# Kernel optimization log

Hardware: AMD Instinct MI355X
Metric: run time of the kernel (lower is better)

The kernel has to match this reference:

```python
import jax, jax.numpy as jnp
import numpy as np

B, T, V = 4, 2048, 2048
D, H, L = 512, 8, 4
HD = D // H


def setup_inputs() -> dict:
    key = jax.random.key(0)
    ks = jax.random.split(key, 8)
    inp = {
        "x": jax.random.normal(ks[0], (B, T, V), dtype=jnp.float32),
        "token_embedding": jax.random.normal(ks[1], (D, V), dtype=jnp.float32),
        "position_embedding": jax.random.normal(ks[2], (T, D), dtype=jnp.float32),
        "Wk": jax.random.normal(ks[3], (L, D, D), dtype=jnp.float32),
        "Wq": jax.random.normal(ks[4], (L, D, D), dtype=jnp.float32),
        "Wv": jax.random.normal(ks[5], (L, D, D), dtype=jnp.float32),
        "Wp": jax.random.normal(ks[6], (L, D, D), dtype=jnp.float32),
        "readout": jax.random.normal(ks[7], (V, D), dtype=jnp.float32),
    }
    return inp


def _attention_block(h, wk, wq, wv, wp):
    # h: [B, T, D]; weights [D, D] (inner_dim == D since head_dim*num_heads == D)
    b, t, c = h.shape
    s = c ** (-0.5)

    def proj(w):
        # F.linear(h, w) = h @ w.T -> [B,T,D] -> [B,H,T,HD], scaled by C^{-1/2}
        return (jnp.einsum('btc,dc->btd', h, w) * s).reshape(b, t, H, HD).transpose(0, 2, 1, 3)

    q, k, v = proj(wq), proj(wk), proj(wv)
    scores = jnp.einsum('bhqd,bhkd->bhqk', q, k) * (HD ** (-0.5))  # [B,H,T,T]
    attn = jax.nn.softmax(scores, axis=-1)
    out = jnp.einsum('bhqk,bhkd->bhqd', attn, v)  # [B,H,T,HD]
    out = out.transpose(0, 2, 1, 3).reshape(b, t, c)
    # projection.size(-1) == inner_dim == D
    return jnp.einsum('btc,oc->bto', out, wp) * (c ** (-0.5))


def reference(x, token_embedding, position_embedding, Wk, Wq, Wv, Wp, readout):
    b, t, c = x.shape  # c == vocab_size
    tok = jnp.einsum('btv,dv->btd', x, token_embedding) * (c ** (-0.5))
    h = tok + position_embedding[:t]
    for l in range(L):
        h = _attention_block(h, Wk[l], Wq[l], Wv[l], Wp[l])
    # logits on last token; readout.size(-1) == D
    logits = jnp.einsum('bd,vd->bv', h[:, -1, :], readout) * (D ** (-0.5))
    return logits
```

## Files before the change

### kernel.cpp

```cpp
#include <hip/hip_runtime.h>
#include <math.h>

typedef __attribute__((ext_vector_type(4))) float    f32x4;
typedef __attribute__((ext_vector_type(2))) _Float16 f16x2;
typedef __attribute__((ext_vector_type(4))) _Float16 f16x4;
typedef __attribute__((ext_vector_type(8))) _Float16 f16x8;

constexpr int Bc  = 4;
constexpr int Tc  = 2048;
constexpr int Vc  = 2048;
constexpr int Dc  = 512;
constexpr int Hc  = 8;
constexpr int HDc = 64;
constexpr int Lc  = 4;
constexpr size_t SZe = (size_t)Bc * Tc * Dc;

constexpr float SM_C = 12.0f;

__device__ __forceinline__ void gload_lds16(const _Float16* g, _Float16* s) {
    __builtin_amdgcn_global_load_lds(
        (const __attribute__((address_space(1))) void*)g,
        (__attribute__((address_space(3))) void*)s,
        16, 0, 0);
}

__device__ __forceinline__ f16x2 cvt_pk(float a, float b) {
    return __builtin_bit_cast(f16x2, __builtin_amdgcn_cvt_pkrtz(a, b));
}

__global__ __launch_bounds__(256) void cvt_k(
    const float* __restrict__ in, _Float16* __restrict__ out, int n4)
{
    for (int i = blockIdx.x * 256 + threadIdx.x; i < n4; i += gridDim.x * 256) {
        float4 v = ((const float4*)in)[i];
        f16x4 h = {(_Float16)v.x, (_Float16)v.y, (_Float16)v.z, (_Float16)v.w};
        *(f16x4*)&out[(size_t)i * 4] = h;
    }
}

__global__ __launch_bounds__(256) void cvtW_k(
    const float* __restrict__ a, const float* __restrict__ b,
    const float* __restrict__ c, const float* __restrict__ d,
    _Float16* __restrict__ oa, _Float16* __restrict__ ob,
    _Float16* __restrict__ oc, _Float16* __restrict__ od, int n4)
{
    const float* in; _Float16* out;
    switch (blockIdx.y) {
        case 0:  in = a; out = oa; break;
        case 1:  in = b; out = ob; break;
        case 2:  in = c; out = oc; break;
        default: in = d; out = od; break;
    }
    for (int i = blockIdx.x * 256 + threadIdx.x; i < n4; i += gridDim.x * 256) {
        float4 v = ((const float4*)in)[i];
        f16x4 h = {(_Float16)v.x, (_Float16)v.y, (_Float16)v.z, (_Float16)v.w};
        *(f16x4*)&out[(size_t)i * 4] = h;
    }
}

template<bool QKV>
__global__ __launch_bounds__(256) void gemm_f16(
    const _Float16* __restrict__ A,
    const _Float16* __restrict__ W0, const _Float16* __restrict__ W1,
    const _Float16* __restrict__ W2,
    void* __restrict__ C0, const float* __restrict__ pos,
    int K, float scA, float scB)
{
    __shared__ __align__(16) _Float16 LA[2][128 * 64];
    __shared__ __align__(16) _Float16 LB[2][128 * 64];

    const int tid = threadIdx.x;
    const int w  = tid >> 6, l = tid & 63;
    const int li = l & 15,  lg = l >> 4;
    const int wm = w >> 1,  wn = w & 1;
    const int m0 = blockIdx.x * 128;

    int sec = 0, n0;
    const _Float16* Wb;
    if (QKV) {
        sec = blockIdx.y >> 2; n0 = (blockIdx.y & 3) * 128;
        Wb = (sec == 0) ? W0 : ((sec == 1) ? W1 : W2);
    } else {
        n0 = blockIdx.y * 128; Wb = W0;
    }
    const float scale = (sec == 0) ? scA : scB;

    const _Float16* srcA[4];
    const _Float16* srcB[4];
#pragma unroll
    for (int i = 0; i < 4; ++i) {
        const int d = i * 4096 + tid * 16;
        const int r = d >> 7, cb = (d & 127) ^ ((r & 7) << 4);
        srcA[i] = A  + (size_t)(m0 + r) * K + (cb >> 1);
        srcB[i] = Wb + (size_t)(n0 + r) * K + (cb >> 1);
    }

    auto stage = [&](int b) {
#pragma unroll
        for (int i = 0; i < 4; ++i) { gload_lds16(srcA[i], &LA[b][i * 2048 + tid * 8]); srcA[i] += 64; }
#pragma unroll
        for (int i = 0; i < 4; ++i) { gload_lds16(srcB[i], &LB[b][i * 2048 + tid * 8]); srcB[i] += 64; }
    };

    f32x4 acc[4][4];
#pragma unroll
    for (int i = 0; i < 4; ++i)
#pragma unroll
        for (int j = 0; j < 4; ++j) acc[i][j] = (f32x4){0.f, 0.f, 0.f, 0.f};

    auto compute = [&](int b) {
        const char* Ab = (const char*)&LA[b][0];
        const char* Bb = (const char*)&LB[b][0];
        f16x8 af[4][2], bf[4][2];
#pragma unroll
        for (int mb = 0; mb < 4; ++mb) {
            const int row = wm * 64 + mb * 16 + li, sz = (row & 7) << 4;
#pragma unroll
            for (int fi = 0; fi < 2; ++fi)
                af[mb][fi] = *(const f16x8*)(Ab + row * 128 + ((fi * 64 + lg * 16) ^ sz));
        }
#pragma unroll
        for (int nb = 0; nb < 4; ++nb) {
            const int row = wn * 64 + nb * 16 + li, sz = (row & 7) << 4;
#pragma unroll
            for (int fi = 0; fi < 2; ++fi)
                bf[nb][fi] = *(const f16x8*)(Bb + row * 128 + ((fi * 64 + lg * 16) ^ sz));
        }
#pragma unroll
        for (int mb = 0; mb < 4; ++mb)
#pragma unroll
            for (int nb = 0; nb < 4; ++nb)
#pragma unroll
                for (int fi = 0; fi < 2; ++fi)
                    acc[mb][nb] = __builtin_amdgcn_mfma_f32_16x16x32_f16(
                        af[mb][fi], bf[nb][fi], acc[mb][nb], 0, 0, 0);
    };

    const int NTk = K >> 6;
    stage(0);
    for (int kt = 0; kt < NTk; ++kt) {
        const int cur = kt & 1;
        if (kt + 1 < NTk) {
            stage(cur ^ 1);
            asm volatile("s_waitcnt vmcnt(8)" ::: "memory");
        } else {
            asm volatile("s_waitcnt vmcnt(0)" ::: "memory");
        }
        __builtin_amdgcn_s_barrier();
        __builtin_amdgcn_sched_barrier(0);
        compute(cur);
        __builtin_amdgcn_s_barrier();
        __builtin_amdgcn_sched_barrier(0);
    }

#pragma unroll
    for (int mb = 0; mb < 4; ++mb) {
#pragma unroll
        for (int nb = 0; nb < 4; ++nb) {
            const int mbase = m0 + wm * 64 + mb * 16 + lg * 4;
            const int nc    = n0 + wn * 64 + nb * 16 + li;
            if (QKV && sec == 2) {
                const int bb2 = mbase >> 11, t0 = mbase & (Tc - 1);
                const int hh2 = nc >> 6,     dd = nc & 63;
                f16x4 vv;
#pragma unroll
                for (int r = 0; r < 4; ++r) vv[r] = (_Float16)(acc[mb][nb][r] * scale);
                _Float16* vt = (_Float16*)C0 + 2 * SZe;
                *(f16x4*)&vt[(((size_t)bb2 * Hc + hh2) * HDc + dd) * Tc + t0] = vv;
            } else if (QKV) {
                _Float16* outp = (_Float16*)C0 + (size_t)sec * SZe;
#pragma unroll
                for (int r = 0; r < 4; ++r) {
                    const int m = mbase + r, bb2 = m >> 11, t = m & (Tc - 1);
                    outp[(((size_t)bb2 * Hc + (nc >> 6)) * Tc + t) * HDc + (nc & 63)] =
                        (_Float16)(acc[mb][nb][r] * scale);
                }
            } else {
                _Float16* outp = (_Float16*)C0;
#pragma unroll
                for (int r = 0; r < 4; ++r) {
                    const int m = mbase + r;
                    float val = acc[mb][nb][r] * scale;
                    if (pos) val += pos[(size_t)(m & (Tc - 1)) * Dc + nc];
                    outp[(size_t)m * Dc + nc] = (_Float16)val;
                }
            }
        }
    }
}

__global__ __launch_bounds__(256) void attn_mfma(
    const _Float16* __restrict__ Qh, const _Float16* __restrict__ Kh,
    const _Float16* __restrict__ Vt, _Float16* __restrict__ o)
{
    __shared__ __align__(16) _Float16 Ks[2][64 * 64];
    __shared__ __align__(16) _Float16 Vs[2][64 * 64];

    const int bid = blockIdx.x;
    const int bh  = bid & 31;
    const int qt  = bid >> 5;
    const int hh  = bh & (Hc - 1);
    const int bb  = bh >> 3;
    const int w   = threadIdx.x >> 6;
    const int l   = threadIdx.x & 63;
    const int li  = l & 15, lg = l >> 4;
    const int q0  = qt * 64 + w * 16;
    const int swz = (li & 7) << 4;

    const _Float16* Qb = Qh + (size_t)bh * Tc * HDc;
    const _Float16* Kb = Kh + (size_t)bh * Tc * HDc;
    const _Float16* Vb = Vt + (size_t)bh * HDc * Tc;

    f16x8 qf[2];
#pragma unroll
    for (int fi = 0; fi < 2; ++fi)
        qf[fi] = *(const f16x8*)&Qb[(size_t)(q0 + li) * HDc + fi * 32 + lg * 8];

    const int off0 = w * 2048 + l * 16;
    const int off1 = off0 + 1024;
    const int r0 = off0 >> 7, cs0 = (off0 & 127) ^ ((r0 & 7) << 4);
    const int r1 = off1 >> 7, cs1 = (off1 & 127) ^ ((r1 & 7) << 4);
    const _Float16* sK0 = Kb + r0 * HDc + (cs0 >> 1);
    const _Float16* sK1 = Kb + r1 * HDc + (cs1 >> 1);
    const _Float16* sV0 = Vb + (size_t)r0 * Tc + (cs0 >> 1);
    const _Float16* sV1 = Vb + (size_t)r1 * Tc + (cs1 >> 1);

    auto stage = [&](int b) {
        gload_lds16(sK0, &Ks[b][w * 1024]);
        gload_lds16(sK1, &Ks[b][w * 1024 + 512]);
        gload_lds16(sV0, &Vs[b][w * 1024]);
        gload_lds16(sV1, &Vs[b][w * 1024 + 512]);
        sK0 += 64 * HDc; sK1 += 64 * HDc;
        sV0 += 64;       sV1 += 64;
    };

    f32x4 oacc[4];
#pragma unroll
    for (int dt = 0; dt < 4; ++dt) oacc[dt] = (f32x4){0.f, 0.f, 0.f, 0.f};
    f32x4 lacc = (f32x4){0.f, 0.f, 0.f, 0.f};
    const f16x4 ones = (f16x4){(_Float16)1.f, (_Float16)1.f, (_Float16)1.f, (_Float16)1.f};

    stage(0);
    constexpr int NT = Tc / 64;
    for (int kt = 0; kt < NT; ++kt) {
        const int cur = kt & 1;
        if (kt + 1 < NT) {
            stage(cur ^ 1);
            asm volatile("s_waitcnt vmcnt(4)" ::: "memory");
        } else {
            asm volatile("s_waitcnt vmcnt(0)" ::: "memory");
        }
        __builtin_amdgcn_s_barrier();
        __builtin_amdgcn_sched_barrier(0);

        const char* KL = (const char*)&Ks[cur][0];
        const char* VL = (const char*)&Vs[cur][0];

        f32x4 s[4];
        __builtin_amdgcn_s_setprio(1);
#pragma unroll
        for (int t = 0; t < 4; ++t) {
            s[t] = (f32x4){-SM_C, -SM_C, -SM_C, -SM_C};
            const char* kr = KL + (t * 16 + li) * 128;
#pragma unroll
            for (int fi = 0; fi < 2; ++fi) {
                f16x8 kf = *(const f16x8*)(kr + ((fi * 64 + lg * 16) ^ swz));
                s[t] = __builtin_amdgcn_mfma_f32_16x16x32_f16(kf, qf[fi], s[t], 0, 0, 0);
            }
        }
        __builtin_amdgcn_s_setprio(0);

        f16x4 pf[4];
#pragma unroll
        for (int t = 0; t < 4; ++t) {
            float p0 = __builtin_amdgcn_exp2f(s[t][0]);
            float p1 = __builtin_amdgcn_exp2f(s[t][1]);
            float p2 = __builtin_amdgcn_exp2f(s[t][2]);
            float p3 = __builtin_amdgcn_exp2f(s[t][3]);
            f16x2 lo = cvt_pk(p0, p1);
            f16x2 hi = cvt_pk(p2, p3);
            pf[t] = (f16x4){lo[0], lo[1], hi[0], hi[1]};
        }

        __builtin_amdgcn_s_setprio(1);
#pragma unroll
        for (int t = 0; t < 4; ++t)
            lacc = __builtin_amdgcn_mfma_f32_16x16x16f16(ones, pf[t], lacc, 0, 0, 0);
#pragma unroll
        for (int dt = 0; dt < 4; ++dt) {
            const char* vr = VL + (dt * 16 + li) * 128;
#pragma unroll
            for (int t = 0; t < 4; ++t) {
                f16x4 vf = *(const f16x4*)(vr + ((t * 32 + lg * 8) ^ swz));
                oacc[dt] = __builtin_amdgcn_mfma_f32_16x16x16f16(vf, pf[t], oacc[dt], 0, 0, 0);
            }
        }
        __builtin_amdgcn_s_setprio(0);

        __builtin_amdgcn_s_barrier();
        __builtin_amdgcn_sched_barrier(0);
    }

    const float inv = 1.f / lacc[0];
    _Float16* op = o + ((size_t)(bb * Tc + q0 + li) * Dc + hh * HDc + lg * 4);
#pragma unroll
    for (int dt = 0; dt < 4; ++dt) {
        f16x4 rv = {(_Float16)(oacc[dt][0] * inv), (_Float16)(oacc[dt][1] * inv),
                    (_Float16)(oacc[dt][2] * inv), (_Float16)(oacc[dt][3] * inv)};
        *(f16x4*)(op + dt * 16) = rv;
    }
}

__global__ __launch_bounds__(256) void readout_k(
    const _Float16* __restrict__ h, const float* __restrict__ ro,
    float* __restrict__ out, float scale)
{
    const int idx = blockIdx.x * 256 + threadIdx.x;
    const int vv  = idx & (Vc - 1);
    const int bb  = idx >> 11;
    const _Float16* hp = h + (size_t)(bb * Tc + (Tc - 1)) * Dc;
    const float* rp = ro + (size_t)vv * Dc;
    float ax = 0.f, ay = 0.f, az = 0.f, aw = 0.f;
#pragma unroll 8
    for (int i = 0; i < Dc / 4; ++i) {
        f16x4  hv = *(const f16x4*)(hp + i * 4);
        float4 rv = *(const float4*)(rp + i * 4);
        ax = fmaf((float)hv[0], rv.x, ax);
        ay = fmaf((float)hv[1], rv.y, ay);
        az = fmaf((float)hv[2], rv.z, az);
        aw = fmaf((float)hv[3], rv.w, aw);
    }
    out[idx] = ((ax + ay) + (az + aw)) * scale;
}

extern "C" void kernel_launch(void* const* d_in, const int* in_sizes, int n_in,
                              void* d_out, int out_size, void* d_ws, size_t ws_size,
                              hipStream_t stream)
{
    const float* x    = (const float*)d_in[0];
    const float* temb = (const float*)d_in[1];
    const float* pemb = (const float*)d_in[2];
    const float* Wk   = (const float*)d_in[3];
    const float* Wq   = (const float*)d_in[4];
    const float* Wv   = (const float*)d_in[5];
    const float* Wp   = (const float*)d_in[6];
    const float* ro   = (const float*)d_in[7];
    float* out = (float*)d_out;

    _Float16* h16    = (_Float16*)d_ws;
    _Float16* temb16 = h16 + SZe;
    _Float16* wq16   = temb16 + (size_t)Dc * Vc;
    _Float16* wk16   = wq16 + (size_t)Lc * Dc * Dc;
    _Float16* wv16   = wk16 + (size_t)Lc * Dc * Dc;
    _Float16* wp16   = wv16 + (size_t)Lc * Dc * Dc;
    _Float16* o16    = wp16 + (size_t)Lc * Dc * Dc;
    _Float16* qh     = o16 + SZe;
    _Float16* kh     = qh + SZe;
    _Float16* vt     = kh + SZe;
    _Float16* x16    = o16;

    const float s_emb  = 1.0f / sqrtf((float)Vc);
    const float s_proj = 1.0f / sqrtf((float)Dc);
    const float s_q    = s_proj * 0.125f * 1.44269504f;

    const int W4 = Lc * Dc * Dc / 4;
    cvt_k<<<2048, 256, 0, stream>>>(x, x16, (int)SZe);
    cvt_k<<<512, 256, 0, stream>>>(temb, temb16, Dc * Vc / 4);
    cvtW_k<<<dim3(512, 4), 256, 0, stream>>>(Wq, Wk, Wv, Wp,
                                             wq16, wk16, wv16, wp16, W4);

    gemm_f16<false><<<dim3(64, 4), 256, 0, stream>>>(
        x16, temb16, nullptr, nullptr, h16, pemb, Vc, s_emb, s_emb);

    const size_t WOFF = (size_t)Dc * Dc;
    for (int lyr = 0; lyr < Lc; ++lyr) {
        gemm_f16<true><<<dim3(64, 12), 256, 0, stream>>>(
            h16, wq16 + lyr * WOFF, wk16 + lyr * WOFF, wv16 + lyr * WOFF,
            qh, nullptr, Dc, s_q, s_proj);

        attn_mfma<<<Bc * Hc * (Tc / 64), 256, 0, stream>>>(qh, kh, vt, o16);

        gemm_f16<false><<<dim3(64, 4), 256, 0, stream>>>(
            o16, wp16 + lyr * WOFF, nullptr, nullptr, h16, nullptr, Dc, s_proj, s_proj);
    }

    readout_k<<<(Bc * Vc) / 256, 256, 0, stream>>>(h16, ro, out, s_proj);
}
```

Baseline: 454.3 us.

## Store K/V in MFMA-fragment order and shrink GEMM N-tile to 64

The QKV GEMM epilogue now writes K and V directly in a pre-tiled layout that matches the MFMA fragment order, so attention stages contiguous 16-byte chunks into LDS and reads fragments with simple linear offsets, with no XOR swizzle. Each V fragment read is now one 8-wide load split into two MFMA operands. Separately, the GEMM tile shrinks from 128x128 to 128x64, doubling the grid in N to raise occupancy and block count. The smaller tile gives less reuse per block, and the scattered scalar K stores in the epilogue may coalesce less well.

Result: faster. 409.9 us (-9.8%).

```diff
diff --git a/kernel.cpp b/kernel.cpp
--- a/kernel.cpp
+++ b/kernel.cpp
@@ -58,6 +58,7 @@
     }
 }
 
+
 template<bool QKV>
 __global__ __launch_bounds__(256) void gemm_f16(
     const _Float16* __restrict__ A,
@@ -67,7 +68,7 @@
     int K, float scA, float scB)
 {
     __shared__ __align__(16) _Float16 LA[2][128 * 64];
-    __shared__ __align__(16) _Float16 LB[2][128 * 64];
+    __shared__ __align__(16) _Float16 LB[2][64 * 64];
 
     const int tid = threadIdx.x;
     const int w  = tid >> 6, l = tid & 63;
@@ -78,20 +79,25 @@
     int sec = 0, n0;
     const _Float16* Wb;
     if (QKV) {
-        sec = blockIdx.y >> 2; n0 = (blockIdx.y & 3) * 128;
+        sec = blockIdx.y >> 3; n0 = (blockIdx.y & 7) * 64;
         Wb = (sec == 0) ? W0 : ((sec == 1) ? W1 : W2);
     } else {
-        n0 = blockIdx.y * 128; Wb = W0;
+        n0 = blockIdx.y * 64; Wb = W0;
     }
     const float scale = (sec == 0) ? scA : scB;
 
     const _Float16* srcA[4];
-    const _Float16* srcB[4];
+    const _Float16* srcB[2];
 #pragma unroll
     for (int i = 0; i < 4; ++i) {
         const int d = i * 4096 + tid * 16;
         const int r = d >> 7, cb = (d & 127) ^ ((r & 7) << 4);
-        srcA[i] = A  + (size_t)(m0 + r) * K + (cb >> 1);
+        srcA[i] = A + (size_t)(m0 + r) * K + (cb >> 1);
+    }
+#pragma unroll
+    for (int i = 0; i < 2; ++i) {
+        const int d = i * 4096 + tid * 16;
+        const int r = d >> 7, cb = (d & 127) ^ ((r & 7) << 4);
         srcB[i] = Wb + (size_t)(n0 + r) * K + (cb >> 1);
     }
 
@@ -99,19 +105,19 @@
 #pragma unroll
         for (int i = 0; i < 4; ++i) { gload_lds16(srcA[i], &LA[b][i * 2048 + tid * 8]); srcA[i] += 64; }
 #pragma unroll
-        for (int i = 0; i < 4; ++i) { gload_lds16(srcB[i], &LB[b][i * 2048 + tid * 8]); srcB[i] += 64; }
+        for (int i = 0; i < 2; ++i) { gload_lds16(srcB[i], &LB[b][i * 2048 + tid * 8]); srcB[i] += 64; }
     };
 
-    f32x4 acc[4][4];
+    f32x4 acc[4][2];
 #pragma unroll
     for (int i = 0; i < 4; ++i)
 #pragma unroll
-        for (int j = 0; j < 4; ++j) acc[i][j] = (f32x4){0.f, 0.f, 0.f, 0.f};
+        for (int j = 0; j < 2; ++j) acc[i][j] = (f32x4){0.f, 0.f, 0.f, 0.f};
 
     auto compute = [&](int b) {
         const char* Ab = (const char*)&LA[b][0];
         const char* Bb = (const char*)&LB[b][0];
-        f16x8 af[4][2], bf[4][2];
+        f16x8 af[4][2], bf[2][2];
 #pragma unroll
         for (int mb = 0; mb < 4; ++mb) {
             const int row = wm * 64 + mb * 16 + li, sz = (row & 7) << 4;
@@ -120,8 +126,8 @@
                 af[mb][fi] = *(const f16x8*)(Ab + row * 128 + ((fi * 64 + lg * 16) ^ sz));
         }
 #pragma unroll
-        for (int nb = 0; nb < 4; ++nb) {
-            const int row = wn * 64 + nb * 16 + li, sz = (row & 7) << 4;
+        for (int nb = 0; nb < 2; ++nb) {
+            const int row = wn * 32 + nb * 16 + li, sz = (row & 7) << 4;
 #pragma unroll
             for (int fi = 0; fi < 2; ++fi)
                 bf[nb][fi] = *(const f16x8*)(Bb + row * 128 + ((fi * 64 + lg * 16) ^ sz));
@@ -129,7 +135,7 @@
 #pragma unroll
         for (int mb = 0; mb < 4; ++mb)
 #pragma unroll
-            for (int nb = 0; nb < 4; ++nb)
+            for (int nb = 0; nb < 2; ++nb)
 #pragma unroll
                 for (int fi = 0; fi < 2; ++fi)
                     acc[mb][nb] = __builtin_amdgcn_mfma_f32_16x16x32_f16(
@@ -142,7 +148,7 @@
         const int cur = kt & 1;
         if (kt + 1 < NTk) {
             stage(cur ^ 1);
-            asm volatile("s_waitcnt vmcnt(8)" ::: "memory");
+            asm volatile("s_waitcnt vmcnt(6)" ::: "memory");
         } else {
             asm volatile("s_waitcnt vmcnt(0)" ::: "memory");
         }
@@ -156,19 +162,32 @@
 #pragma unroll
     for (int mb = 0; mb < 4; ++mb) {
 #pragma unroll
-        for (int nb = 0; nb < 4; ++nb) {
+        for (int nb = 0; nb < 2; ++nb) {
             const int mbase = m0 + wm * 64 + mb * 16 + lg * 4;
-            const int nc    = n0 + wn * 64 + nb * 16 + li;
+            const int nc    = n0 + wn * 32 + nb * 16 + li;
             if (QKV && sec == 2) {
-                const int bb2 = mbase >> 11, t0 = mbase & (Tc - 1);
-                const int hh2 = nc >> 6,     dd = nc & 63;
+                const int t = mbase & (Tc - 1);
+                const int bh2 = (mbase >> 11) * Hc + (nc >> 6), d = nc & 63;
                 f16x4 vv;
 #pragma unroll
                 for (int r = 0; r < 4; ++r) vv[r] = (_Float16)(acc[mb][nb][r] * scale);
-                _Float16* vt = (_Float16*)C0 + 2 * SZe;
-                *(f16x4*)&vt[(((size_t)bb2 * Hc + hh2) * HDc + dd) * Tc + t0] = vv;
+                _Float16* vf = (_Float16*)C0 + 2 * SZe;
+                const size_t adr =
+                    (((size_t)bh2 * 32 + (t >> 6)) * 8 + ((d >> 4) & 3) * 2 + ((t >> 5) & 1)) * 512
+                    + ((d & 15) + 16 * ((t >> 2) & 3)) * 8 + ((t >> 4) & 1) * 4;
+                *(f16x4*)&vf[adr] = vv;
+            } else if (QKV && sec == 1) {
+                _Float16* kf = (_Float16*)C0 + SZe;
+                const int t0 = mbase & (Tc - 1);
+                const int bh2 = (mbase >> 11) * Hc + (nc >> 6), d = nc & 63;
+                const size_t adr0 =
+                    (((size_t)bh2 * 32 + (t0 >> 6)) * 8 + ((t0 >> 4) & 3) * 2 + (d >> 5)) * 512
+                    + ((t0 & 15) + 16 * ((d >> 3) & 3)) * 8 + (d & 7);
+#pragma unroll
+                for (int r = 0; r < 4; ++r)
+                    kf[adr0 + (size_t)r * 8] = (_Float16)(acc[mb][nb][r] * scale);
             } else if (QKV) {
-                _Float16* outp = (_Float16*)C0 + (size_t)sec * SZe;
+                _Float16* outp = (_Float16*)C0;
 #pragma unroll
                 for (int r = 0; r < 4; ++r) {
                     const int m = mbase + r, bb2 = m >> 11, t = m & (Tc - 1);
@@ -190,48 +209,41 @@
 }
 
 __global__ __launch_bounds__(256) void attn_mfma(
-    const _Float16* __restrict__ Qh, const _Float16* __restrict__ Kh,
-    const _Float16* __restrict__ Vt, _Float16* __restrict__ o)
-{
-    __shared__ __align__(16) _Float16 Ks[2][64 * 64];
-    __shared__ __align__(16) _Float16 Vs[2][64 * 64];
+    const _Float16* __restrict__ Qh, const _Float16* __restrict__ Kf,
+    const _Float16* __restrict__ Vf, _Float16* __restrict__ o)
+{
+    __shared__ __align__(16) _Float16 Ks[2][4096];
+    __shared__ __align__(16) _Float16 Vs[2][4096];
 
     const int bid = blockIdx.x;
     const int bh  = bid & 31;
     const int qt  = bid >> 5;
     const int hh  = bh & (Hc - 1);
     const int bb  = bh >> 3;
-    const int w   = threadIdx.x >> 6;
-    const int l   = threadIdx.x & 63;
+    const int tid = threadIdx.x;
+    const int w   = tid >> 6;
+    const int l   = tid & 63;
     const int li  = l & 15, lg = l >> 4;
     const int q0  = qt * 64 + w * 16;
-    const int swz = (li & 7) << 4;
 
     const _Float16* Qb = Qh + (size_t)bh * Tc * HDc;
-    const _Float16* Kb = Kh + (size_t)bh * Tc * HDc;
-    const _Float16* Vb = Vt + (size_t)bh * HDc * Tc;
 
     f16x8 qf[2];
 #pragma unroll
     for (int fi = 0; fi < 2; ++fi)
         qf[fi] = *(const f16x8*)&Qb[(size_t)(q0 + li) * HDc + fi * 32 + lg * 8];
 
-    const int off0 = w * 2048 + l * 16;
-    const int off1 = off0 + 1024;
-    const int r0 = off0 >> 7, cs0 = (off0 & 127) ^ ((r0 & 7) << 4);
-    const int r1 = off1 >> 7, cs1 = (off1 & 127) ^ ((r1 & 7) << 4);
-    const _Float16* sK0 = Kb + r0 * HDc + (cs0 >> 1);
-    const _Float16* sK1 = Kb + r1 * HDc + (cs1 >> 1);
-    const _Float16* sV0 = Vb + (size_t)r0 * Tc + (cs0 >> 1);
-    const _Float16* sV1 = Vb + (size_t)r1 * Tc + (cs1 >> 1);
+    const _Float16* sK0 = Kf + (size_t)bh * Tc * HDc + tid * 8;
+    const _Float16* sK1 = sK0 + 2048;
+    const _Float16* sV0 = Vf + (size_t)bh * Tc * HDc + tid * 8;
+    const _Float16* sV1 = sV0 + 2048;
 
     auto stage = [&](int b) {
-        gload_lds16(sK0, &Ks[b][w * 1024]);
-        gload_lds16(sK1, &Ks[b][w * 1024 + 512]);
-        gload_lds16(sV0, &Vs[b][w * 1024]);
-        gload_lds16(sV1, &Vs[b][w * 1024 + 512]);
-        sK0 += 64 * HDc; sK1 += 64 * HDc;
-        sV0 += 64;       sV1 += 64;
+        gload_lds16(sK0, &Ks[b][tid * 8]);
+        gload_lds16(sK1, &Ks[b][2048 + tid * 8]);
+        gload_lds16(sV0, &Vs[b][tid * 8]);
+        gload_lds16(sV1, &Vs[b][2048 + tid * 8]);
+        sK0 += 4096; sK1 += 4096; sV0 += 4096; sV1 += 4096;
     };
 
     f32x4 oacc[4];
@@ -253,19 +265,18 @@
         __builtin_amdgcn_s_barrier();
         __builtin_amdgcn_sched_barrier(0);
 
-        const char* KL = (const char*)&Ks[cur][0];
-        const char* VL = (const char*)&Vs[cur][0];
+        const _Float16* KL = &Ks[cur][0];
+        const _Float16* VL = &Vs[cur][0];
 
         f32x4 s[4];
         __builtin_amdgcn_s_setprio(1);
 #pragma unroll
         for (int t = 0; t < 4; ++t) {
             s[t] = (f32x4){-SM_C, -SM_C, -SM_C, -SM_C};
-            const char* kr = KL + (t * 16 + li) * 128;
 #pragma unroll
             for (int fi = 0; fi < 2; ++fi) {
-                f16x8 kf = *(const f16x8*)(kr + ((fi * 64 + lg * 16) ^ swz));
-                s[t] = __builtin_amdgcn_mfma_f32_16x16x32_f16(kf, qf[fi], s[t], 0, 0, 0);
+                f16x8 kfr = *(const f16x8*)(KL + (t * 2 + fi) * 512 + l * 8);
+                s[t] = __builtin_amdgcn_mfma_f32_16x16x32_f16(kfr, qf[fi], s[t], 0, 0, 0);
             }
         }
         __builtin_amdgcn_s_setprio(0);
@@ -288,11 +299,13 @@
             lacc = __builtin_amdgcn_mfma_f32_16x16x16f16(ones, pf[t], lacc, 0, 0, 0);
 #pragma unroll
         for (int dt = 0; dt < 4; ++dt) {
-            const char* vr = VL + (dt * 16 + li) * 128;
-#pragma unroll
-            for (int t = 0; t < 4; ++t) {
-                f16x4 vf = *(const f16x4*)(vr + ((t * 32 + lg * 8) ^ swz));
-                oacc[dt] = __builtin_amdgcn_mfma_f32_16x16x16f16(vf, pf[t], oacc[dt], 0, 0, 0);
+#pragma unroll
+            for (int m = 0; m < 2; ++m) {
+                f16x8 vv = *(const f16x8*)(VL + (dt * 2 + m) * 512 + l * 8);
+                f16x4 vlo = (f16x4){vv[0], vv[1], vv[2], vv[3]};
+                f16x4 vhi = (f16x4){vv[4], vv[5], vv[6], vv[7]};
+                oacc[dt] = __builtin_amdgcn_mfma_f32_16x16x16f16(vlo, pf[2 * m],     oacc[dt], 0, 0, 0);
+                oacc[dt] = __builtin_amdgcn_mfma_f32_16x16x16f16(vhi, pf[2 * m + 1], oacc[dt], 0, 0, 0);
             }
         }
         __builtin_amdgcn_s_setprio(0);
@@ -355,8 +368,8 @@
     _Float16* wp16   = wv16 + (size_t)Lc * Dc * Dc;
     _Float16* o16    = wp16 + (size_t)Lc * Dc * Dc;
     _Float16* qh     = o16 + SZe;
-    _Float16* kh     = qh + SZe;
-    _Float16* vt     = kh + SZe;
+    _Float16* khF    = qh + SZe;
+    _Float16* vhF    = khF + SZe;
     _Float16* x16    = o16;
 
     const float s_emb  = 1.0f / sqrtf((float)Vc);
@@ -369,18 +382,18 @@
     cvtW_k<<<dim3(512, 4), 256, 0, stream>>>(Wq, Wk, Wv, Wp,
                                              wq16, wk16, wv16, wp16, W4);
 
-    gemm_f16<false><<<dim3(64, 4), 256, 0, stream>>>(
+    gemm_f16<false><<<dim3(64, 8), 256, 0, stream>>>(
         x16, temb16, nullptr, nullptr, h16, pemb, Vc, s_emb, s_emb);
 
     const size_t WOFF = (size_t)Dc * Dc;
     for (int lyr = 0; lyr < Lc; ++lyr) {
-        gemm_f16<true><<<dim3(64, 12), 256, 0, stream>>>(
+        gemm_f16<true><<<dim3(64, 24), 256, 0, stream>>>(
             h16, wq16 + lyr * WOFF, wk16 + lyr * WOFF, wv16 + lyr * WOFF,
             qh, nullptr, Dc, s_q, s_proj);
 
-        attn_mfma<<<Bc * Hc * (Tc / 64), 256, 0, stream>>>(qh, kh, vt, o16);
-
-        gemm_f16<false><<<dim3(64, 4), 256, 0, stream>>>(
+        attn_mfma<<<Bc * Hc * (Tc / 64), 256, 0, stream>>>(qh, khF, vhF, o16);
+
+        gemm_f16<false><<<dim3(64, 8), 256, 0, stream>>>(
             o16, wp16 + lyr * WOFF, nullptr, nullptr, h16, nullptr, Dc, s_proj, s_proj);
     }
 
```
